# Kernel optimization log

Measured on AMD Instinct MI355X. Metric: run time of the kernel, lower is better.

Reference implementation:

```python
import jax, jax.numpy as jnp
import numpy as np

N, K, D = 131072, 1024, 128
COMMITMENT_COST = 0.25


def setup_inputs() -> dict:
    key = jax.random.key(0)
    k1, k2 = jax.random.split(key)
    c_input = jax.random.normal(k1, (N, D), dtype=jnp.float32)
    # nn.Embedding weight initialized N(0, 0.1)
    embedding_weight = jax.random.normal(k2, (K, D), dtype=jnp.float32) * 0.1
    return {"c_input": c_input, "embedding_weight": embedding_weight}


def reference(c_input, embedding_weight):
    distances = (
        jnp.sum(c_input ** 2, axis=1, keepdims=True)
        + jnp.sum(embedding_weight ** 2, axis=1)
        - 2.0 * jnp.matmul(c_input, embedding_weight.T)
    )
    encoding_indices = jnp.argmin(distances, axis=1)  # [N]
    encodings = jax.nn.one_hot(encoding_indices, K, dtype=c_input.dtype)  # [N, K]
    # one-hot @ weight == direct gather
    quantized = embedding_weight[encoding_indices]  # [N, D]
    e_latent_loss = jnp.mean((jax.lax.stop_gradient(quantized) - c_input) ** 2)
    q_latent_loss = jnp.mean((quantized - jax.lax.stop_gradient(c_input)) ** 2)
    loss = q_latent_loss + COMMITMENT_COST * e_latent_loss
    # straight-through estimator
    quantized_st = c_input + jax.lax.stop_gradient(quantized - c_input)
    return (loss, quantized_st, encodings)
```

## Files before the change

### kernel.cpp

```cpp
#include <hip/hip_runtime.h>
#include <hip/hip_bf16.h>

#define NROWS 131072
#define KC 1024
#define DD 128
#define MARGIN 1e-3f

typedef __attribute__((ext_vector_type(8))) short short8;
typedef __attribute__((ext_vector_type(4))) float f32x4;
typedef __attribute__((ext_vector_type(2))) float f32x2;

__device__ inline short f2bf_hi(float f) {
  unsigned u = __builtin_bit_cast(unsigned, f);
  u += 0x7fffu + ((u >> 16) & 1u);
  return (short)(u >> 16);
}
__device__ inline float bf2f(short s) {
  unsigned u = ((unsigned)(unsigned short)s) << 16;
  return __builtin_bit_cast(float, u);
}

__global__ void vq_prep(const float* __restrict__ E, short* __restrict__ EH,
                        short* __restrict__ EL, float* __restrict__ SE,
                        float* __restrict__ out) {
  int b = blockIdx.x, t = threadIdx.x;
  if (b < 64) {
    int idx = b * 256 + t;
    int s = (idx >> 6) & 3, l = idx & 63;
    int c = idx >> 8;
    int q = l >> 4, n = l & 15;
    const float* src = E + (16 * c + n) * DD + 32 * s + 8 * q;
    short8 h, lo;
#pragma unroll
    for (int j = 0; j < 8; ++j) {
      float x = src[j];
      short hb = f2bf_hi(x);
      h[j] = hb;
      lo[j] = f2bf_hi(x - bf2f(hb));
    }
    *(short8*)(EH + idx * 8) = h;
    *(short8*)(EL + idx * 8) = lo;
  } else {
    if (t == 0) out[0] = 0.f;
    for (int k = t; k < KC; k += 256) {
      double acc = 0.0;
      const float* er = E + k * DD;
      for (int i = 0; i < DD; ++i) { double v = (double)er[i]; acc += v * v; }
      SE[k] = (float)acc;
    }
  }
}

__global__ __launch_bounds__(256, 4) void vq_main(
    const float* __restrict__ X, const float* __restrict__ E,
    const short* __restrict__ EH, const short* __restrict__ EL,
    const float* __restrict__ SE, float* __restrict__ out) {
  __shared__ __align__(16) short lbh[8192];
  __shared__ __align__(16) short lbl[8192];
  __shared__ __align__(16) float lse[KC];
  __shared__ int lidx[128];
  __shared__ int lflag[128];
  __shared__ int lany;
  __shared__ float lx[128];
  __shared__ float lrv[4];
  __shared__ int lri[4];
  __shared__ float lsx;
  __shared__ float lloss[4];

  const int tid = threadIdx.x;
  const int w = tid >> 6, l = tid & 63, q = l >> 4, n = l & 15;
  const int row_base = blockIdx.x * 128;
  const int rot = blockIdx.x & 15;
  const int encb = 1 + NROWS * DD;
  if (tid == 0) lany = 0;
  *(f32x4*)(lse + tid * 4) = *(const f32x4*)(SE + tid * 4);

  float* zb = out + encb + row_base * KC;
  if (tid < 3) __builtin_nontemporal_store(0.f, zb + tid);
  else if (tid == 3) __builtin_nontemporal_store(0.f, zb + 131071);
  float* zb4 = zb + 3;

  short8 ah[2][4], al[2][4];
#pragma unroll
  for (int mt = 0; mt < 2; ++mt) {
    const float* xp = X + (row_base + 32 * w + 16 * mt + n) * DD + 8 * q;
#pragma unroll
    for (int s = 0; s < 4; ++s) {
      f32x4 x0 = *(const f32x4*)(xp + 32 * s);
      f32x4 x1 = *(const f32x4*)(xp + 32 * s + 4);
#pragma unroll
      for (int j = 0; j < 4; ++j) {
        short hb = f2bf_hi(x0[j]);
        ah[mt][s][j] = hb;
        al[mt][s][j] = f2bf_hi(x0[j] - bf2f(hb));
        short hb2 = f2bf_hi(x1[j]);
        ah[mt][s][j + 4] = hb2;
        al[mt][s][j + 4] = f2bf_hi(x1[j] - bf2f(hb2));
      }
    }
  }

  float bestv[8], secv[8];
  int besti[8];
#pragma unroll
  for (int i = 0; i < 8; ++i) { bestv[i] = -3e38f; secv[i] = -3e38f; besti[i] = 0; }

  const f32x4 z4 = {0.f, 0.f, 0.f, 0.f};
  for (int cc = 0; cc < 16; ++cc) {
    const int ccr = (cc + rot) & 15;
    {
      const short8* gh = (const short8*)(EH + ccr * 8192);
      const short8* gl = (const short8*)(EL + ccr * 8192);
      short8* dh = (short8*)lbh;
      short8* dl = (short8*)lbl;
#pragma unroll
      for (int i = 0; i < 4; ++i) {
        int u = i * 256 + tid;
        dh[u] = gh[u];
        dl[u] = gl[u];
      }
    }
    __syncthreads();

#pragma unroll
    for (int u2 = 0; u2 < 8; ++u2) {
      int j = cc * 2048 + u2 * 256 + tid;
      if (j < 32767) __builtin_nontemporal_store(z4, (f32x4*)(zb4 + 4 * j));
    }
    __builtin_amdgcn_sched_barrier(0);

#pragma unroll
    for (int nt = 0; nt < 4; ++nt) {
      f32x4 a0 = {0.f, 0.f, 0.f, 0.f}, a1 = {0.f, 0.f, 0.f, 0.f};
#pragma unroll
      for (int s = 0; s < 4; ++s) {
        short8 bh  = *(const short8*)(lbh + ((nt * 4 + s) * 64 + l) * 8);
        short8 blo = *(const short8*)(lbl + ((nt * 4 + s) * 64 + l) * 8);
        a0 = __builtin_amdgcn_mfma_f32_16x16x32_bf16(ah[0][s], bh,  a0, 0, 0, 0);
        a1 = __builtin_amdgcn_mfma_f32_16x16x32_bf16(ah[1][s], bh,  a1, 0, 0, 0);
        a0 = __builtin_amdgcn_mfma_f32_16x16x32_bf16(al[0][s], bh,  a0, 0, 0, 0);
        a1 = __builtin_amdgcn_mfma_f32_16x16x32_bf16(al[1][s], bh,  a1, 0, 0, 0);
        a0 = __builtin_amdgcn_mfma_f32_16x16x32_bf16(ah[0][s], blo, a0, 0, 0, 0);
        a1 = __builtin_amdgcn_mfma_f32_16x16x32_bf16(ah[1][s], blo, a1, 0, 0, 0);
      }
      int k = ccr * 64 + nt * 16 + n;
      float hse = 0.5f * lse[k];
#pragma unroll
      for (int r = 0; r < 4; ++r) {
        {
          float sc = a0[r] - hse;
          bool gt = sc > bestv[r];
          secv[r] = gt ? bestv[r] : fmaxf(secv[r], sc);
          if (gt) { bestv[r] = sc; besti[r] = k; }
        }
        {
          int sl = 4 + r;
          float sc = a1[r] - hse;
          bool gt = sc > bestv[sl];
          secv[sl] = gt ? bestv[sl] : fmaxf(secv[sl], sc);
          if (gt) { bestv[sl] = sc; besti[sl] = k; }
        }
      }
    }
    __syncthreads();
  }

#pragma unroll
  for (int slot = 0; slot < 8; ++slot) {
    float v = bestv[slot], s2 = secv[slot];
    int bi = besti[slot];
#pragma unroll
    for (int m = 1; m <= 8; m <<= 1) {
      float v2 = __shfl_xor(v, m, 64);
      float sv2 = __shfl_xor(s2, m, 64);
      int i2 = __shfl_xor(bi, m, 64);
      float ns = fmaxf(fminf(v, v2), fmaxf(s2, sv2));
      if (v2 > v || (v2 == v && i2 < bi)) { v = v2; bi = i2; }
      s2 = ns;
    }
    if (n == 0) {
      int mt = slot >> 2, r = slot & 3;
      int rl = 32 * w + 16 * mt + 4 * q + r;
      int f = (v - s2) <= MARGIN;
      lidx[rl] = bi;
      lflag[rl] = f;
      if (f) lany = 1;
    }
  }
  __syncthreads();

  if (lany) {
    for (int rl = 0; rl < 128; ++rl) {
      if (lflag[rl] == 0) continue;
      if (tid < DD) lx[tid] = X[(row_base + rl) * DD + tid];
      __syncthreads();
      if (tid < 64) {
        double v0 = lx[tid], v1 = lx[tid + 64];
        double s = v0 * v0 + v1 * v1;
#pragma unroll
        for (int m = 1; m < 64; m <<= 1) s += __shfl_xor(s, m, 64);
        if (tid == 0) lsx = (float)s;
      }
      __syncthreads();
      float dmin = 3e38f; int kmin = 0;
      for (int kk = tid; kk < KC; kk += 256) {
        double dot = 0.0;
        const float* er = E + kk * DD;
        for (int i = 0; i < DD; ++i) dot += (double)lx[i] * (double)er[i];
        float a = lsx + lse[kk];
        float b2 = (float)(2.0 * dot);
        float dnp = a - b2;
        if (dnp < dmin) { dmin = dnp; kmin = kk; }
      }
#pragma unroll
      for (int m = 1; m < 64; m <<= 1) {
        float v2 = __shfl_xor(dmin, m, 64);
        int k2 = __shfl_xor(kmin, m, 64);
        if (v2 < dmin || (v2 == dmin && k2 < kmin)) { dmin = v2; kmin = k2; }
      }
      if (l == 0) { lrv[w] = dmin; lri[w] = kmin; }
      __syncthreads();
      if (tid == 0) {
        float dm = lrv[0]; int km = lri[0];
#pragma unroll
        for (int t2 = 1; t2 < 4; ++t2)
          if (lrv[t2] < dm || (lrv[t2] == dm && lri[t2] < km)) { dm = lrv[t2]; km = lri[t2]; }
        lidx[rl] = km;
      }
      __syncthreads();
    }
  }
  __syncthreads();

  float lp = 0.f;
  for (int rl = w; rl < 128; rl += 4) {
    int row = row_base + rl;
    int idx = lidx[rl];
    f32x2 xv = *(const f32x2*)(X + row * DD + 2 * l);
    f32x2 ev = *(const f32x2*)(E + idx * DD + 2 * l);
    float d0 = ev[0] - xv[0], d1 = ev[1] - xv[1];
    __builtin_nontemporal_store(xv[0] + d0, out + 1 + row * DD + 2 * l);
    __builtin_nontemporal_store(xv[1] + d1, out + 1 + row * DD + 2 * l + 1);
    lp += d0 * d0 + d1 * d1;
    if (l == (idx & 63)) out[encb + row * KC + idx] = 1.f;
  }
#pragma unroll
  for (int m = 1; m < 64; m <<= 1) lp += __shfl_xor(lp, m, 64);
  if (l == 0) lloss[w] = lp;
  __syncthreads();
  if (tid == 0) {
    float t = (lloss[0] + lloss[1] + lloss[2] + lloss[3]) *
              (1.25f / ((float)NROWS * (float)DD));
    atomicAdd(out, t);
  }
}

extern "C" void kernel_launch(void* const* d_in, const int* in_sizes, int n_in,
                              void* d_out, int out_size, void* d_ws, size_t ws_size,
                              hipStream_t stream) {
  const float* X = (const float*)d_in[0];
  const float* E = (const float*)d_in[1];
  float* out = (float*)d_out;
  short* EH = (short*)d_ws;
  short* EL = EH + KC * DD;
  float* SE = (float*)(EL + KC * DD);
  vq_prep<<<65, 256, 0, stream>>>(E, EH, EL, SE, out);
  vq_main<<<NROWS / 128, 256, 0, stream>>>(X, E, EH, EL, SE, out);
}
```

Baseline: 788.1 us.

## Split argmin and output writing into separate kernels

Moves the 512 MB one-hot zero-fill and the quantized/loss output out of the MFMA argmin kernel into a new output kernel, with indices passed through a workspace buffer. The argmin kernel no longer interleaves nontemporal stores with its matrix work, and the output kernel can stream stores at full bandwidth. This gives up the overlap of compute and store traffic that the fused kernel had, and adds a launch plus an index round trip through memory.

```diff
diff --git a/kernel.cpp b/kernel.cpp
--- a/kernel.cpp
+++ b/kernel.cpp
@@ -51,10 +51,10 @@
   }
 }
 
-__global__ __launch_bounds__(256, 4) void vq_main(
+__global__ __launch_bounds__(256, 4) void vq_argmin(
     const float* __restrict__ X, const float* __restrict__ E,
     const short* __restrict__ EH, const short* __restrict__ EL,
-    const float* __restrict__ SE, float* __restrict__ out) {
+    const float* __restrict__ SE, int* __restrict__ IDX) {
   __shared__ __align__(16) short lbh[8192];
   __shared__ __align__(16) short lbl[8192];
   __shared__ __align__(16) float lse[KC];
@@ -65,20 +65,13 @@
   __shared__ float lrv[4];
   __shared__ int lri[4];
   __shared__ float lsx;
-  __shared__ float lloss[4];
 
   const int tid = threadIdx.x;
   const int w = tid >> 6, l = tid & 63, q = l >> 4, n = l & 15;
   const int row_base = blockIdx.x * 128;
   const int rot = blockIdx.x & 15;
-  const int encb = 1 + NROWS * DD;
   if (tid == 0) lany = 0;
   *(f32x4*)(lse + tid * 4) = *(const f32x4*)(SE + tid * 4);
-
-  float* zb = out + encb + row_base * KC;
-  if (tid < 3) __builtin_nontemporal_store(0.f, zb + tid);
-  else if (tid == 3) __builtin_nontemporal_store(0.f, zb + 131071);
-  float* zb4 = zb + 3;
 
   short8 ah[2][4], al[2][4];
 #pragma unroll
@@ -105,7 +98,6 @@
 #pragma unroll
   for (int i = 0; i < 8; ++i) { bestv[i] = -3e38f; secv[i] = -3e38f; besti[i] = 0; }
 
-  const f32x4 z4 = {0.f, 0.f, 0.f, 0.f};
   for (int cc = 0; cc < 16; ++cc) {
     const int ccr = (cc + rot) & 15;
     {
@@ -121,13 +113,6 @@
       }
     }
     __syncthreads();
-
-#pragma unroll
-    for (int u2 = 0; u2 < 8; ++u2) {
-      int j = cc * 2048 + u2 * 256 + tid;
-      if (j < 32767) __builtin_nontemporal_store(z4, (f32x4*)(zb4 + 4 * j));
-    }
-    __builtin_amdgcn_sched_barrier(0);
 
 #pragma unroll
     for (int nt = 0; nt < 4; ++nt) {
@@ -232,6 +217,22 @@
   }
   __syncthreads();
 
+  if (tid < 128) IDX[row_base + tid] = lidx[tid];
+}
+
+__global__ __launch_bounds__(256) void vq_out(
+    const float* __restrict__ X, const float* __restrict__ E,
+    const int* __restrict__ IDX, float* __restrict__ out) {
+  __shared__ int lidx[128];
+  __shared__ float lloss[4];
+  const int tid = threadIdx.x;
+  const int w = tid >> 6, l = tid & 63;
+  const int row_base = blockIdx.x * 128;
+  const int encb = 1 + NROWS * DD;
+
+  if (tid < 128) lidx[tid] = IDX[row_base + tid];
+  __syncthreads();
+
   float lp = 0.f;
   for (int rl = w; rl < 128; rl += 4) {
     int row = row_base + rl;
@@ -242,8 +243,25 @@
     __builtin_nontemporal_store(xv[0] + d0, out + 1 + row * DD + 2 * l);
     __builtin_nontemporal_store(xv[1] + d1, out + 1 + row * DD + 2 * l + 1);
     lp += d0 * d0 + d1 * d1;
+  }
+
+  float* zb = out + encb + row_base * KC;
+  if (tid < 3) __builtin_nontemporal_store(0.f, zb + tid);
+  else if (tid == 3) __builtin_nontemporal_store(0.f, zb + 131071);
+  float* zb4 = zb + 3;
+  const f32x4 z4 = {0.f, 0.f, 0.f, 0.f};
+  for (int u = 0; u < 127; ++u)
+    __builtin_nontemporal_store(z4, (f32x4*)(zb4 + 4 * (u * 256 + tid)));
+  if (tid < 255)
+    __builtin_nontemporal_store(z4, (f32x4*)(zb4 + 4 * (127 * 256 + tid)));
+  __syncthreads();
+
+  for (int rl = w; rl < 128; rl += 4) {
+    int row = row_base + rl;
+    int idx = lidx[rl];
     if (l == (idx & 63)) out[encb + row * KC + idx] = 1.f;
   }
+
 #pragma unroll
   for (int m = 1; m < 64; m <<= 1) lp += __shfl_xor(lp, m, 64);
   if (l == 0) lloss[w] = lp;
@@ -264,6 +282,8 @@
   short* EH = (short*)d_ws;
   short* EL = EH + KC * DD;
   float* SE = (float*)(EL + KC * DD);
+  int* IDX = (int*)(SE + KC);
   vq_prep<<<65, 256, 0, stream>>>(E, EH, EL, SE, out);
-  vq_main<<<NROWS / 128, 256, 0, stream>>>(X, E, EH, EL, SE, out);
-}
+  vq_argmin<<<NROWS / 128, 256, 0, stream>>>(X, E, EH, EL, SE, IDX);
+  vq_out<<<NROWS / 128, 256, 0, stream>>>(X, E, IDX, out);
+}
```

New measurement: 889.8 us. 1.13x slower.
